# Performance work log

Measured on AMD Instinct MI355X. Metric: run time of the kernel, lower is better.

## Reference

```python
import jax, jax.numpy as jnp
import numpy as np
import math

EMBED_DIM = 768
NUM_HEADS = 12
HEAD_DIM = EMBED_DIM // NUM_HEADS
SPARSITY = 0.1


def setup_inputs() -> dict:
    key = jax.random.key(0)
    ks = jax.random.split(key, 5)
    B, N, D = 4, 1024, EMBED_DIM
    s = 1.0 / math.sqrt(D)
    return {
        "x": jax.random.normal(ks[0], (B, N, D), dtype=jnp.float32),
        "W_qkv": jax.random.normal(ks[1], (D, 3 * D), dtype=jnp.float32) * s,
        "b_qkv": jnp.zeros((3 * D,), dtype=jnp.float32),
        "W_out": jax.random.normal(ks[2], (D, D), dtype=jnp.float32) * s,
        "b_out": jnp.zeros((D,), dtype=jnp.float32),
    }


def reference(x, W_qkv, b_qkv, W_out, b_out):
    B, N, D = x.shape
    H, hd = NUM_HEADS, HEAD_DIM
    qkv = x @ W_qkv + b_qkv                      # [B,N,3D]
    qkv = qkv.reshape(B, N, 3, H, hd).transpose(2, 0, 3, 1, 4)  # [3,B,H,N,hd]
    q, k, v = qkv[0], qkv[1], qkv[2]
    attn = jnp.einsum("bhqd,bhkd->bhqk", q, k) * (1.0 / math.sqrt(hd))  # [B,H,N,N]
    kth = int(N * N * SPARSITY)
    if kth > 0:
        # kth smallest value over the flattened per-(b,h) attention matrix
        flat = attn.reshape(B, H, N * N)
        thr = jnp.sort(flat, axis=-1)[..., kth - 1]               # [B,H]
        attn = jnp.where(attn <= thr[:, :, None, None], -1e9, attn)
    attn = jax.nn.softmax(attn, axis=-1)
    out = jnp.einsum("bhqk,bhkd->bhqd", attn, v)                  # [B,H,N,hd]
    out = out.transpose(0, 2, 1, 3).reshape(B, N, D)
    return out @ W_out + b_out
```

## Files before the change

### kernel.cpp

```cpp
#include <hip/hip_runtime.h>
#include <math.h>

#define SEQ 1024
#define DMODEL 768
#define NHEADS 12
#define HDIM 64
#define D3 2304
#define BH 48
#define NTOK 4096
#define KTH 104857u
#define NBIN 4096
#define BIN0 14336

typedef __bf16 bf16x8 __attribute__((ext_vector_type(8)));
typedef float  f32x4  __attribute__((ext_vector_type(4)));

#define SWZ(row, chunk) ((row) * 32 + (((chunk) ^ (((row) >> 1) & 3)) * 8))

__device__ __forceinline__ void gl16(const ushort* g, ushort* l) {
    __builtin_amdgcn_global_load_lds(
        (__attribute__((address_space(1))) void*)(size_t)(g),
        (__attribute__((address_space(3))) void*)(l), 16, 0, 0);
}

__device__ __forceinline__ void split1(float x, ushort& h, ushort& l) {
    unsigned b  = __float_as_uint(x);
    unsigned hb = (b + 0x7FFFu + ((b >> 16) & 1u)) >> 16;
    float hf = __uint_as_float(hb << 16);
    float r  = x - hf;
    unsigned rb = __float_as_uint(r);
    unsigned lb = (rb + 0x7FFFu + ((rb >> 16) & 1u)) >> 16;
    h = (ushort)hb; l = (ushort)lb;
}

__device__ __forceinline__ ushort bf16rne(float x) {
    unsigned b = __float_as_uint(x);
    return (ushort)((b + 0x7FFFu + ((b >> 16) & 1u)) >> 16);
}

__global__ __launch_bounds__(256) void k_xsplit(const float* __restrict__ x,
                                                ushort* __restrict__ xh,
                                                ushort* __restrict__ xl, int n,
                                                unsigned* __restrict__ hist) {
    int g = blockIdx.x * 256 + threadIdx.x;
    if (g < BH * NBIN) hist[g] = 0u;
    int i = g * 4;
    if (i >= n) return;
    float4 v = *(const float4*)(x + i);
    ushort4 h, l;
    split1(v.x, h.x, l.x); split1(v.y, h.y, l.y);
    split1(v.z, h.z, l.z); split1(v.w, h.w, l.w);
    *(ushort4*)(xh + i) = h;
    *(ushort4*)(xl + i) = l;
}

__global__ __launch_bounds__(256) void k_wsplit(const float* __restrict__ W,
                                                ushort* __restrict__ Wth,
                                                ushort* __restrict__ Wtl,
                                                int K, int N) {
    __shared__ float t[64][65];
    int k0 = blockIdx.y * 64, n0 = blockIdx.x * 64;
    int tid = threadIdx.x;
    int r = tid >> 4, c = (tid & 15) * 4;
#pragma unroll
    for (int u = 0; u < 4; u++) {
        int rr = r + u * 16;
        float4 v = *(const float4*)(W + (size_t)(k0 + rr) * N + n0 + c);
        t[rr][c] = v.x; t[rr][c + 1] = v.y; t[rr][c + 2] = v.z; t[rr][c + 3] = v.w;
    }
    __syncthreads();
    int n = tid >> 2, kc = (tid & 3) * 16;
    ushort hb[16] __attribute__((aligned(16)));
    ushort lb[16] __attribute__((aligned(16)));
#pragma unroll
    for (int j = 0; j < 16; j++) split1(t[kc + j][n], hb[j], lb[j]);
    ushort* dh = Wth + (size_t)(n0 + n) * K + k0 + kc;
    ushort* dl = Wtl + (size_t)(n0 + n) * K + k0 + kc;
    *(uint4*)(dh)     = *(uint4*)&hb[0];
    *(uint4*)(dh + 8) = *(uint4*)&hb[8];
    *(uint4*)(dl)     = *(uint4*)&lb[0];
    *(uint4*)(dl + 8) = *(uint4*)&lb[8];
}

#define STAGE_LDS(ko)                                                           \
    gl16(gAh + (ko), &sA[0][wbase]);                                            \
    gl16(gAh2 + (ko), &sA[0][2048 + wbase]);                                    \
    gl16(gAl + (ko), &sA[1][wbase]);                                            \
    gl16(gAl2 + (ko), &sA[1][2048 + wbase]);                                    \
    gl16(gBh + (ko), &sB[0][wbase]);                                            \
    gl16(gBh2 + (ko), &sB[0][2048 + wbase]);                                    \
    gl16(gBl + (ko), &sB[1][wbase]);                                            \
    gl16(gBl2 + (ko), &sB[1][2048 + wbase]);

#define GEMM_CORE_SETUP(Kdim)                                                   \
    __shared__ ushort sA[2][128 * 32];                                          \
    __shared__ ushort sB[2][128 * 32];                                          \
    int tid = threadIdx.x, lane = tid & 63, wave = tid >> 6;                    \
    int wm = (wave >> 1) * 64, wn = (wave & 1) * 64;                            \
    int l15 = lane & 15, q = lane >> 4;                                         \
    int sr = tid >> 2, sc = tid & 3;                                            \
    const int K = (Kdim);                                                       \
    int scs = sc ^ ((sr >> 1) & 3);          \
    const ushort* gAh = Ah + (size_t)(m0 + sr) * K + scs * 8;                   \
    const ushort* gAl = Al + (size_t)(m0 + sr) * K + scs * 8;                   \
    const ushort* gBh = Bh + (size_t)(n0 + sr) * K + scs * 8;                   \
    const ushort* gBl = Bl + (size_t)(n0 + sr) * K + scs * 8;                   \
    const ushort* gAh2 = gAh + (size_t)64 * K;                                  \
    const ushort* gAl2 = gAl + (size_t)64 * K;                                  \
    const ushort* gBh2 = gBh + (size_t)64 * K;                                  \
    const ushort* gBl2 = gBl + (size_t)64 * K;                                  \
    int wbase = wave * 512;              \
    f32x4 acc[4][4] = {};                                                       \
    STAGE_LDS(0)                                                                \
    __syncthreads();                                                            \
    const int NIT = K / 32;                                                     \
    for (int it = 0; it < NIT; ++it) {                                          \
        bf16x8 fah[4], fal[4], fbh[4], fbl[4];                                  \
        _Pragma("unroll")                                                       \
        for (int mt = 0; mt < 4; mt++) {                                        \
            int rr = wm + mt * 16 + l15;                                        \
            fah[mt] = *(const bf16x8*)(&sA[0][SWZ(rr, q)]);                     \
            fal[mt] = *(const bf16x8*)(&sA[1][SWZ(rr, q)]);                     \
        }                                                                       \
        _Pragma("unroll")                                                       \
        for (int nt = 0; nt < 4; nt++) {                                        \
            int rr = wn + nt * 16 + l15;                                        \
            fbh[nt] = *(const bf16x8*)(&sB[0][SWZ(rr, q)]);                     \
            fbl[nt] = *(const bf16x8*)(&sB[1][SWZ(rr, q)]);                     \
        }                                                                       \
        __syncthreads();                 \
        if (it + 1 < NIT) { STAGE_LDS((it + 1) * 32) }                          \
        _Pragma("unroll")                                                       \
        for (int mt = 0; mt < 4; mt++)                                          \
            _Pragma("unroll")                                                   \
            for (int nt = 0; nt < 4; nt++) {                                    \
                acc[mt][nt] = __builtin_amdgcn_mfma_f32_16x16x32_bf16(          \
                    fah[mt], fbh[nt], acc[mt][nt], 0, 0, 0);                    \
                acc[mt][nt] = __builtin_amdgcn_mfma_f32_16x16x32_bf16(          \
                    fah[mt], fbl[nt], acc[mt][nt], 0, 0, 0);                    \
                acc[mt][nt] = __builtin_amdgcn_mfma_f32_16x16x32_bf16(          \
                    fal[mt], fbh[nt], acc[mt][nt], 0, 0, 0);                    \
            }                                                                   \
        __syncthreads();                   \
    }

__global__ __launch_bounds__(256) void k_gemm_out(
    const ushort* __restrict__ Ah, const ushort* __restrict__ Al,
    const ushort* __restrict__ Bh, const ushort* __restrict__ Bl,
    const float* __restrict__ bias, float* __restrict__ C,
    int M, int N, int Kin) {
    int m0 = blockIdx.y * 128, n0 = blockIdx.x * 128;
    GEMM_CORE_SETUP(Kin)
#pragma unroll
    for (int nt = 0; nt < 4; nt++) {
        int col = n0 + wn + nt * 16 + l15;
        float bv = bias[col];
#pragma unroll
        for (int mt = 0; mt < 4; mt++) {
            int rowb = m0 + wm + mt * 16 + q * 4;
#pragma unroll
            for (int r = 0; r < 4; r++)
                C[(size_t)(rowb + r) * N + col] = acc[mt][nt][r] + bv;
        }
    }
}

__global__ __launch_bounds__(256) void k_gemm_qkv(
    const ushort* __restrict__ Ah, const ushort* __restrict__ Al,
    const ushort* __restrict__ Bh, const ushort* __restrict__ Bl,
    const float* __restrict__ bias,
    ushort* __restrict__ Qh, ushort* __restrict__ Ql,
    ushort* __restrict__ Kh, ushort* __restrict__ Kl,
    ushort* __restrict__ Vth) {
    int m0 = blockIdx.y * 128, n0 = blockIdx.x * 128;
    GEMM_CORE_SETUP(DMODEL)
    int region = n0 / 768;
#pragma unroll
    for (int nt = 0; nt < 4; nt++) {
        int col = n0 + wn + nt * 16 + l15;
        float bv = bias[col];
        int cin = col - region * 768;
        int h = cin >> 6, d = cin & 63;
#pragma unroll
        for (int mt = 0; mt < 4; mt++) {
            int rowb = m0 + wm + mt * 16 + q * 4;
            int b = rowb >> 10;
            int s0 = rowb & 1023;
            int bh = b * NHEADS + h;
            if (region == 2) {
                ushort h4[4] __attribute__((aligned(8)));
#pragma unroll
                for (int r = 0; r < 4; r++)
                    h4[r] = bf16rne(acc[mt][nt][r] + bv);
                size_t off = ((size_t)(bh * 64 + d) << 10) + s0;
                *(ushort4*)(Vth + off) = *(ushort4*)h4;
            } else {
                ushort* Ph = region ? Kh : Qh;
                ushort* Pl = region ? Kl : Ql;
                size_t off = ((size_t)((bh << 10) + s0)) * 64 + d;
#pragma unroll
                for (int r = 0; r < 4; r++) {
                    ushort hs, ls;
                    split1(acc[mt][nt][r] + bv, hs, ls);
                    Ph[off + (size_t)r * 64] = hs;
                    Pl[off + (size_t)r * 64] = ls;
                }
            }
        }
    }
}

__global__ __launch_bounds__(256) void k_scores(
    const ushort* __restrict__ Qh, const ushort* __restrict__ Ql,
    const ushort* __restrict__ Kh, const ushort* __restrict__ Kl,
    unsigned* __restrict__ hist) {
    __shared__ unsigned lh[NBIN];
    int orig = blockIdx.x;
    int wid = (orig & 7) * 384 + (orig >> 3);
    int bh = wid >> 6;
    int rem = wid & 63;
    int i0 = (rem >> 3) * 128, j0 = (rem & 7) * 128;
    int tid = threadIdx.x, lane = tid & 63, wave = tid >> 6;
    int l15 = lane & 15, q = lane >> 4;
    int wj = (wave >> 1) * 64, wi = (wave & 1) * 64;
    for (int i = tid; i < NBIN; i += 256) lh[i] = 0u;
    __syncthreads();

    const ushort* qb  = Qh + ((size_t)bh << 16);
    const ushort* qlb = Ql + ((size_t)bh << 16);
    const ushort* kb  = Kh + ((size_t)bh << 16);
    const ushort* klb = Kl + ((size_t)bh << 16);

    bf16x8 fqh[4][2], fql[4][2];
#pragma unroll
    for (int nt = 0; nt < 4; nt++)
#pragma unroll
        for (int kk = 0; kk < 2; kk++) {
            size_t off = (size_t)(i0 + wi + nt * 16 + l15) * 64 + kk * 32 + q * 8;
            fqh[nt][kk] = *(const bf16x8*)(qb + off);
            fql[nt][kk] = *(const bf16x8*)(qlb + off);
        }
    bf16x8 fkh[2][2], fkl[2][2];
#pragma unroll
    for (int kk = 0; kk < 2; kk++) {
        size_t off = (size_t)(j0 + wj + l15) * 64 + kk * 32 + q * 8;
        fkh[0][kk] = *(const bf16x8*)(kb + off);
        fkl[0][kk] = *(const bf16x8*)(klb + off);
    }

#pragma unroll
    for (int mt = 0; mt < 4; mt++) {
        int cur = mt & 1;
        if (mt < 3) {
            int nxt = cur ^ 1;
#pragma unroll
            for (int kk = 0; kk < 2; kk++) {
                size_t off = (size_t)(j0 + wj + (mt + 1) * 16 + l15) * 64 + kk * 32 + q * 8;
                fkh[nxt][kk] = *(const bf16x8*)(kb + off);
                fkl[nxt][kk] = *(const bf16x8*)(klb + off);
            }
        }
        f32x4 acc[4] = {};
#pragma unroll
        for (int kk = 0; kk < 2; kk++)
#pragma unroll
            for (int nt = 0; nt < 4; nt++) {
                acc[nt] = __builtin_amdgcn_mfma_f32_16x16x32_bf16(
                    fkh[cur][kk], fqh[nt][kk], acc[nt], 0, 0, 0);
                acc[nt] = __builtin_amdgcn_mfma_f32_16x16x32_bf16(
                    fkl[cur][kk], fqh[nt][kk], acc[nt], 0, 0, 0);
                acc[nt] = __builtin_amdgcn_mfma_f32_16x16x32_bf16(
                    fkh[cur][kk], fql[nt][kk], acc[nt], 0, 0, 0);
            }
#pragma unroll
        for (int nt = 0; nt < 4; nt++) {
#pragma unroll
            for (int r = 0; r < 4; r++) {
                ushort u = bf16rne(__expf(acc[nt][r] * 0.125f));
                int bin = (int)u - BIN0;
                bin = (bin < 0) ? 0 : ((bin > NBIN - 1) ? NBIN - 1 : bin);
                atomicAdd(&lh[bin], 1u);
            }
        }
    }
    __syncthreads();
    for (int i = tid; i < NBIN; i += 256) {
        unsigned cc = lh[i];
        if (cc) atomicAdd(&hist[bh * NBIN + i], cc);
    }
}

__global__ __launch_bounds__(256) void k_pv(const ushort* __restrict__ Qh,
                                            const ushort* __restrict__ Ql,
                                            const ushort* __restrict__ Kh,
                                            const ushort* __restrict__ Kl,
                                            const ushort* __restrict__ Vth,
                                            const unsigned* __restrict__ hist,
                                            ushort* __restrict__ ctxh,
                                            ushort* __restrict__ ctxl) {
    __shared__ ushort sK[2][2][32 * 64];
    __shared__ ushort sV[2][64 * 32];
    __shared__ ushort pt[4][32 * 40] __attribute__((aligned(16)));
    __shared__ unsigned ps[256];
    __shared__ unsigned thrS;
    int orig = blockIdx.x;
    int wid = (orig & 7) * 48 + (orig >> 3);
    int bh = wid >> 3;
    int i0 = (wid & 7) * 128;
    int b = bh / NHEADS, h = bh % NHEADS;
    int tid = threadIdx.x, lane = tid & 63, wave = tid >> 6;
    int l15 = lane & 15, q = lane >> 4;

    const ushort* qb  = Qh + ((size_t)bh << 16);
    const ushort* qlb = Ql + ((size_t)bh << 16);
    const ushort* kb  = Kh + ((size_t)bh << 16);
    const ushort* klb = Kl + ((size_t)bh << 16);
    const ushort* vh0 = Vth + ((size_t)bh << 16);

    int sr2 = tid >> 3, sc2 = tid & 7;
    const ushort* gK  = kb  + (size_t)sr2 * 64 + ((sc2 ^ (sr2 & 7)) * 8);
    const ushort* gKl = klb + (size_t)sr2 * 64 + ((sc2 ^ (sr2 & 7)) * 8);
    int sr = tid >> 2, sc = tid & 3;
    const ushort* gV = vh0 + (size_t)sr * 1024 + ((sc ^ ((sr >> 1) & 3)) * 8);
    int wbase = wave * 512;

    gl16(gK,  &sK[0][0][wbase]);
    gl16(gKl, &sK[0][1][wbase]);
    gl16(gV,  &sV[0][wbase]);

    const unsigned* hrow = hist + bh * NBIN;
    unsigned psum = 0;
#pragma unroll
    for (int i = 0; i < 16; i++) psum += hrow[tid * 16 + i];
    ps[tid] = psum;
    __syncthreads();
    unsigned pre = 0;
    for (int u = 0; u < 256; u++) {
        unsigned v = ps[u];
        if (u < tid) pre += v;
    }
    if (pre < KTH && pre + psum >= KTH) {
        unsigned run = pre; int d = 15;
#pragma unroll
        for (int i = 0; i < 16; i++) {
            unsigned v = hrow[tid * 16 + i];
            if (run + v >= KTH) { d = i; break; }
            run += v;
        }
        thrS = (unsigned)(BIN0 + tid * 16 + d);
    }
    __syncthreads();
    unsigned t = thrS;

    bf16x8 fqh[2][2], fql[2][2];
#pragma unroll
    for (int ig = 0; ig < 2; ig++)
#pragma unroll
        for (int kk = 0; kk < 2; kk++) {
            size_t off = (size_t)(i0 + wave * 32 + ig * 16 + l15) * 64 + kk * 32 + q * 8;
            fqh[ig][kk] = *(const bf16x8*)(qb + off);
            fql[ig][kk] = *(const bf16x8*)(qlb + off);
        }

    f32x4 accp[2][4] = {};
    f32x4 lacc[2] = {};
    uint4 onesu = {0x3F803F80u, 0x3F803F80u, 0x3F803F80u, 0x3F803F80u};
    bf16x8 ones = *(bf16x8*)&onesu;
    ushort* myP = &pt[wave][0];

    for (int j0 = 0; j0 < SEQ; j0 += 32) {
        int cur = (j0 >> 5) & 1;
        bf16x8 kh[2][2], kl[2][2];
#pragma unroll
        for (int j16 = 0; j16 < 2; j16++) {
            int row = j16 * 16 + l15, rs = row & 7;
#pragma unroll
            for (int kk = 0; kk < 2; kk++) {
                int off = row * 64 + (((kk * 4 + q) ^ rs) * 8);
                kh[j16][kk] = *(const bf16x8*)(&sK[cur][0][off]);
                kl[j16][kk] = *(const bf16x8*)(&sK[cur][1][off]);
            }
        }
        bf16x8 fvh[4];
#pragma unroll
        for (int nt = 0; nt < 4; nt++)
            fvh[nt] = *(const bf16x8*)(&sV[cur][SWZ(nt * 16 + l15, q)]);
        if (j0 + 32 < SEQ) {
            int nxt = cur ^ 1;
            gl16(gK  + (size_t)(j0 + 32) * 64, &sK[nxt][0][wbase]);
            gl16(gKl + (size_t)(j0 + 32) * 64, &sK[nxt][1][wbase]);
            gl16(gV  + (j0 + 32),              &sV[nxt][wbase]);
        }
        bf16x8 pa[2];
#pragma unroll
        for (int ig = 0; ig < 2; ig++) {
#pragma unroll
            for (int j16 = 0; j16 < 2; j16++) {
                f32x4 s = {};
                s = __builtin_amdgcn_mfma_f32_16x16x32_bf16(kh[j16][0], fqh[ig][0], s, 0, 0, 0);
                s = __builtin_amdgcn_mfma_f32_16x16x32_bf16(kl[j16][0], fqh[ig][0], s, 0, 0, 0);
                s = __builtin_amdgcn_mfma_f32_16x16x32_bf16(kh[j16][0], fql[ig][0], s, 0, 0, 0);
                s = __builtin_amdgcn_mfma_f32_16x16x32_bf16(kh[j16][1], fqh[ig][1], s, 0, 0, 0);
                s = __builtin_amdgcn_mfma_f32_16x16x32_bf16(kl[j16][1], fqh[ig][1], s, 0, 0, 0);
                s = __builtin_amdgcn_mfma_f32_16x16x32_bf16(kh[j16][1], fql[ig][1], s, 0, 0, 0);
                unsigned pb[4];
#pragma unroll
                for (int r = 0; r < 4; r++) {
                    unsigned u = bf16rne(__expf(s[r] * 0.125f));
                    pb[r] = (u <= t) ? 0u : u;
                }
                uint2 w;
                w.x = pb[0] | (pb[1] << 16);
                w.y = pb[2] | (pb[3] << 16);
                *(uint2*)(&myP[(ig * 16 + l15) * 40 + j16 * 16 + q * 4]) = w;
            }
            pa[ig] = *(const bf16x8*)(&myP[(ig * 16 + l15) * 40 + q * 8]);
        }
#pragma unroll
        for (int ig = 0; ig < 2; ig++) {
#pragma unroll
            for (int nt = 0; nt < 4; nt++)
                accp[ig][nt] = __builtin_amdgcn_mfma_f32_16x16x32_bf16(
                    pa[ig], fvh[nt], accp[ig][nt], 0, 0, 0);
            lacc[ig] = __builtin_amdgcn_mfma_f32_16x16x32_bf16(
                pa[ig], ones, lacc[ig], 0, 0, 0);
        }
        __syncthreads();
    }
#pragma unroll
    for (int ig = 0; ig < 2; ig++)
#pragma unroll
        for (int r = 0; r < 4; r++) {
            int i = i0 + wave * 32 + ig * 16 + q * 4 + r;
            float l = lacc[ig][r];
#pragma unroll
            for (int nt = 0; nt < 4; nt++) {
                int d = nt * 16 + l15;
                ushort hs, ls;
                split1(accp[ig][nt][r] / l, hs, ls);
                size_t off = ((size_t)(b * SEQ + i)) * DMODEL + h * 64 + d;
                ctxh[off] = hs;
                ctxl[off] = ls;
            }
        }
}

extern "C" void kernel_launch(void* const* d_in, const int* in_sizes, int n_in,
                              void* d_out, int out_size, void* d_ws, size_t ws_size,
                              hipStream_t stream) {
    const float* x    = (const float*)d_in[0];
    const float* Wqkv = (const float*)d_in[1];
    const float* bqkv = (const float*)d_in[2];
    const float* Wout = (const float*)d_in[3];
    const float* bout = (const float*)d_in[4];
    float* out = (float*)d_out;

    char* ws = (char*)d_ws;
    ushort* Qh  = (ushort*)(ws + 0);
    ushort* Ql  = (ushort*)(ws + 6291456);
    ushort* Kh  = (ushort*)(ws + 12582912);
    ushort* Kl  = (ushort*)(ws + 18874368);
    ushort* Vth = (ushort*)(ws + 25165824);
    ushort* ctxh = (ushort*)(ws + 239075328);
    ushort* ctxl = (ushort*)(ws + 245366784);
    unsigned* hist = (unsigned*)(ws + 251658240);
    ushort* xh     = (ushort*)(ws + 37748736);
    ushort* xl     = (ushort*)(ws + 37748736 + 6291456);
    ushort* Wqkvth = (ushort*)(ws + 37748736 + 12582912);
    ushort* Wqkvtl = (ushort*)(ws + 37748736 + 16121856);
    ushort* Woutth = (ushort*)(ws + 37748736);
    ushort* Wouttl = (ushort*)(ws + 37748736 + 1179648);

    k_xsplit<<<NTOK * DMODEL / 1024, 256, 0, stream>>>(x, xh, xl, NTOK * DMODEL, hist);
    k_wsplit<<<dim3(D3 / 64, DMODEL / 64), 256, 0, stream>>>(Wqkv, Wqkvth, Wqkvtl, DMODEL, D3);
    k_gemm_qkv<<<dim3(D3 / 128, NTOK / 128), 256, 0, stream>>>(
        xh, xl, Wqkvth, Wqkvtl, bqkv, Qh, Ql, Kh, Kl, Vth);
    k_scores<<<3072, 256, 0, stream>>>(Qh, Ql, Kh, Kl, hist);
    k_pv<<<384, 256, 0, stream>>>(Qh, Ql, Kh, Kl, Vth, hist, ctxh, ctxl);
    k_wsplit<<<dim3(DMODEL / 64, DMODEL / 64), 256, 0, stream>>>(Wout, Woutth, Wouttl, DMODEL, DMODEL);
    k_gemm_out<<<dim3(DMODEL / 128, NTOK / 128), 256, 0, stream>>>(
        ctxh, ctxl, Woutth, Wouttl, bout, out, NTOK, DMODEL, DMODEL);
}
```

Baseline: 280.5 us.

## Merge prep kernels and widen score blocks to cover four key tiles

Folds the x split, hist clearing, and both weight split/transpose kernels into one k_prep launch. This cuts launches and lets the Wout transpose run early, so it moves to its own workspace region. k_scores now gives each block 512 key columns instead of 128, 768 blocks instead of 3072. This reuses the Q fragments held in registers and the per-block LDS histogram init and flush across four tiles. Fewer blocks may lower occupancy and load balance.

```diff
diff --git a/kernel.cpp b/kernel.cpp
--- a/kernel.cpp
+++ b/kernel.cpp
@@ -38,29 +38,39 @@
     return (ushort)((b + 0x7FFFu + ((b >> 16) & 1u)) >> 16);
 }
 
-__global__ __launch_bounds__(256) void k_xsplit(const float* __restrict__ x,
-                                                ushort* __restrict__ xh,
-                                                ushort* __restrict__ xl, int n,
-                                                unsigned* __restrict__ hist) {
-    int g = blockIdx.x * 256 + threadIdx.x;
-    if (g < BH * NBIN) hist[g] = 0u;
-    int i = g * 4;
-    if (i >= n) return;
-    float4 v = *(const float4*)(x + i);
-    ushort4 h, l;
-    split1(v.x, h.x, l.x); split1(v.y, h.y, l.y);
-    split1(v.z, h.z, l.z); split1(v.w, h.w, l.w);
-    *(ushort4*)(xh + i) = h;
-    *(ushort4*)(xl + i) = l;
-}
-
-__global__ __launch_bounds__(256) void k_wsplit(const float* __restrict__ W,
-                                                ushort* __restrict__ Wth,
-                                                ushort* __restrict__ Wtl,
-                                                int K, int N) {
+__global__ __launch_bounds__(256) void k_prep(
+    const float* __restrict__ x, ushort* __restrict__ xh,
+    ushort* __restrict__ xl, int n, unsigned* __restrict__ hist,
+    const float* __restrict__ Wqkv, ushort* __restrict__ Wqth,
+    ushort* __restrict__ Wqtl,
+    const float* __restrict__ Wout, ushort* __restrict__ Woth,
+    ushort* __restrict__ Wotl) {
     __shared__ float t[64][65];
-    int k0 = blockIdx.y * 64, n0 = blockIdx.x * 64;
-    int tid = threadIdx.x;
+    int bx = blockIdx.x, tid = threadIdx.x;
+    if (bx < 3072) {
+        int g = bx * 256 + tid;
+        if (g < BH * NBIN) hist[g] = 0u;
+        int i = g * 4;
+        if (i >= n) return;
+        float4 v = *(const float4*)(x + i);
+        ushort4 hh, ll;
+        split1(v.x, hh.x, ll.x); split1(v.y, hh.y, ll.y);
+        split1(v.z, hh.z, ll.z); split1(v.w, hh.w, ll.w);
+        *(ushort4*)(xh + i) = hh;
+        *(ushort4*)(xl + i) = ll;
+        return;
+    }
+    const float* W; ushort* Wth; ushort* Wtl; int N, n0, k0;
+    if (bx < 3504) {
+        int b2 = bx - 3072;
+        W = Wqkv; Wth = Wqth; Wtl = Wqtl; N = D3;
+        n0 = (b2 % 36) * 64; k0 = (b2 / 36) * 64;
+    } else {
+        int b2 = bx - 3504;
+        W = Wout; Wth = Woth; Wtl = Wotl; N = DMODEL;
+        n0 = (b2 % 12) * 64; k0 = (b2 / 12) * 64;
+    }
+    const int K = DMODEL;
     int r = tid >> 4, c = (tid & 15) * 4;
 #pragma unroll
     for (int u = 0; u < 4; u++) {
@@ -69,13 +79,13 @@
         t[rr][c] = v.x; t[rr][c + 1] = v.y; t[rr][c + 2] = v.z; t[rr][c + 3] = v.w;
     }
     __syncthreads();
-    int n = tid >> 2, kc = (tid & 3) * 16;
+    int nn = tid >> 2, kc = (tid & 3) * 16;
     ushort hb[16] __attribute__((aligned(16)));
     ushort lb[16] __attribute__((aligned(16)));
 #pragma unroll
-    for (int j = 0; j < 16; j++) split1(t[kc + j][n], hb[j], lb[j]);
-    ushort* dh = Wth + (size_t)(n0 + n) * K + k0 + kc;
-    ushort* dl = Wtl + (size_t)(n0 + n) * K + k0 + kc;
+    for (int j = 0; j < 16; j++) split1(t[kc + j][nn], hb[j], lb[j]);
+    ushort* dh = Wth + (size_t)(n0 + nn) * K + k0 + kc;
+    ushort* dl = Wtl + (size_t)(n0 + nn) * K + k0 + kc;
     *(uint4*)(dh)     = *(uint4*)&hb[0];
     *(uint4*)(dh + 8) = *(uint4*)&hb[8];
     *(uint4*)(dl)     = *(uint4*)&lb[0];
@@ -216,10 +226,11 @@
     unsigned* __restrict__ hist) {
     __shared__ unsigned lh[NBIN];
     int orig = blockIdx.x;
-    int wid = (orig & 7) * 384 + (orig >> 3);
-    int bh = wid >> 6;
-    int rem = wid & 63;
-    int i0 = (rem >> 3) * 128, j0 = (rem & 7) * 128;
+    int wid = (orig & 7) * 96 + (orig >> 3);
+    int bh = wid >> 4;
+    int rem = wid & 15;
+    int i0 = (rem >> 1) * 128;
+    int j0b = (rem & 1) * 512;
     int tid = threadIdx.x, lane = tid & 63, wave = tid >> 6;
     int l15 = lane & 15, q = lane >> 4;
     int wj = (wave >> 1) * 64, wi = (wave & 1) * 64;
@@ -241,24 +252,25 @@
             fql[nt][kk] = *(const bf16x8*)(qlb + off);
         }
     bf16x8 fkh[2][2], fkl[2][2];
-#pragma unroll
-    for (int kk = 0; kk < 2; kk++) {
-        size_t off = (size_t)(j0 + wj + l15) * 64 + kk * 32 + q * 8;
-        fkh[0][kk] = *(const bf16x8*)(kb + off);
-        fkl[0][kk] = *(const bf16x8*)(klb + off);
-    }
-
-#pragma unroll
-    for (int mt = 0; mt < 4; mt++) {
-        int cur = mt & 1;
-        if (mt < 3) {
-            int nxt = cur ^ 1;
-#pragma unroll
-            for (int kk = 0; kk < 2; kk++) {
-                size_t off = (size_t)(j0 + wj + (mt + 1) * 16 + l15) * 64 + kk * 32 + q * 8;
-                fkh[nxt][kk] = *(const bf16x8*)(kb + off);
-                fkl[nxt][kk] = *(const bf16x8*)(klb + off);
-            }
+    {
+        size_t off = (size_t)(j0b + wj + l15) * 64 + q * 8;
+        fkh[0][0] = *(const bf16x8*)(kb + off);
+        fkl[0][0] = *(const bf16x8*)(klb + off);
+        fkh[0][1] = *(const bf16x8*)(kb + off + 32);
+        fkl[0][1] = *(const bf16x8*)(klb + off + 32);
+    }
+
+#pragma unroll
+    for (int s = 0; s < 16; s++) {
+        int cur = s & 1;
+        if (s + 1 < 16) {
+            int s1 = s + 1;
+            int jr = j0b + (s1 >> 2) * 128 + wj + (s1 & 3) * 16;
+            size_t off = (size_t)(jr + l15) * 64 + q * 8;
+            fkh[cur ^ 1][0] = *(const bf16x8*)(kb + off);
+            fkl[cur ^ 1][0] = *(const bf16x8*)(klb + off);
+            fkh[cur ^ 1][1] = *(const bf16x8*)(kb + off + 32);
+            fkl[cur ^ 1][1] = *(const bf16x8*)(klb + off + 32);
         }
         f32x4 acc[4] = {};
 #pragma unroll
@@ -468,16 +480,15 @@
     ushort* xl     = (ushort*)(ws + 37748736 + 6291456);
     ushort* Wqkvth = (ushort*)(ws + 37748736 + 12582912);
     ushort* Wqkvtl = (ushort*)(ws + 37748736 + 16121856);
-    ushort* Woutth = (ushort*)(ws + 37748736);
-    ushort* Wouttl = (ushort*)(ws + 37748736 + 1179648);
-
-    k_xsplit<<<NTOK * DMODEL / 1024, 256, 0, stream>>>(x, xh, xl, NTOK * DMODEL, hist);
-    k_wsplit<<<dim3(D3 / 64, DMODEL / 64), 256, 0, stream>>>(Wqkv, Wqkvth, Wqkvtl, DMODEL, D3);
+    ushort* Woutth = (ushort*)(ws + 57409536);
+    ushort* Wouttl = (ushort*)(ws + 58589184);
+
+    k_prep<<<3648, 256, 0, stream>>>(x, xh, xl, NTOK * DMODEL, hist,
+                                     Wqkv, Wqkvth, Wqkvtl, Wout, Woutth, Wouttl);
     k_gemm_qkv<<<dim3(D3 / 128, NTOK / 128), 256, 0, stream>>>(
         xh, xl, Wqkvth, Wqkvtl, bqkv, Qh, Ql, Kh, Kl, Vth);
-    k_scores<<<3072, 256, 0, stream>>>(Qh, Ql, Kh, Kl, hist);
+    k_scores<<<768, 256, 0, stream>>>(Qh, Ql, Kh, Kl, hist);
     k_pv<<<384, 256, 0, stream>>>(Qh, Ql, Kh, Kl, Vth, hist, ctxh, ctxl);
-    k_wsplit<<<dim3(DMODEL / 64, DMODEL / 64), 256, 0, stream>>>(Wout, Woutth, Wouttl, DMODEL, DMODEL);
     k_gemm_out<<<dim3(DMODEL / 128, NTOK / 128), 256, 0, stream>>>(
         ctxh, ctxl, Woutth, Wouttl, bout, out, NTOK, DMODEL, DMODEL);
 }
```

Measured after the change: 254.1 us. -9.4%, faster.
